# Kernel tuning notes

Measured on AMD Instinct MI355X. Metric: run time of the kernel, lower is better.

## Reference

```python
import jax, jax.numpy as jnp
import numpy as np

NUM_CLASSES = 21
TOP_K = 200
CONF_THRESH = 0.01
NMS_THRESH = 0.045
VAR0, VAR1 = 0.1, 0.2  # SSD decode variances
B, N = 128, 8732  # batch, num anchors (SSD300)


def setup_inputs() -> dict:
    key = jax.random.key(0)
    k1, k2, k3 = jax.random.split(key, 3)
    loc = jax.random.normal(k1, (B, N, 4), jnp.float32)
    conf = jax.random.normal(k2, (B, N, NUM_CLASSES), jnp.float32)
    # anchors in center-size form (cx, cy, w, h), values in (0,1)
    anchors = jax.random.uniform(k3, (N, 4), jnp.float32)
    return {"loc": loc, "conf": conf, "anchors": anchors}


def decode(loc, anchors):
    # loc [N,4], anchors [N,4] (cx,cy,w,h) -> corner boxes [N,4]
    cxcy = anchors[:, :2] + loc[:, :2] * VAR0 * anchors[:, 2:]
    wh = anchors[:, 2:] * jnp.exp(loc[:, 2:] * VAR1)
    return jnp.concatenate([cxcy - 0.5 * wh, cxcy + 0.5 * wh], axis=-1)


def pairwise_iou(boxes):
    # boxes [K,4] -> IoU [K,K]
    lt = jnp.maximum(boxes[:, None, :2], boxes[None, :, :2])
    rb = jnp.minimum(boxes[:, None, 2:], boxes[None, :, 2:])
    wh = jnp.clip(rb - lt, 0.0)
    inter = wh[..., 0] * wh[..., 1]
    area = (boxes[:, 2] - boxes[:, 0]) * (boxes[:, 3] - boxes[:, 1])
    return inter / (area[:, None] + area[None, :] - inter + 1e-12)


def nms_one_class(scores, boxes):
    # scores [N], boxes [N,4] -> packed [TOP_K, 5] (score, x1,y1,x2,y2)
    masked = jnp.where(scores > CONF_THRESH, scores, 0.0)
    top_s, idx = jax.lax.top_k(masked, TOP_K)
    top_b = boxes[idx]                      # [K,4]
    iou = pairwise_iou(top_b)               # [K,K]
    ar = jnp.arange(TOP_K)
    def body(i, keep):
        sup = keep[i] & (iou[i] > NMS_THRESH) & (ar > i)
        return keep & ~sup
    keep = jax.lax.fori_loop(0, TOP_K, body, top_s > CONF_THRESH)
    # pack kept detections to the front (stable sort preserves score order)
    order = jnp.argsort(jnp.logical_not(keep))
    ent = jnp.concatenate([top_s[:, None], top_b], axis=-1)[order]
    return jnp.where(keep[order][:, None], ent, 0.0)


def reference(loc, conf, anchors):
    probs = jax.nn.softmax(conf, axis=-1)   # [B,N,C]
    def per_image(loc_i, probs_i):
        boxes = decode(loc_i, anchors)      # [N,4]
        return jax.vmap(lambda s: nms_one_class(s, boxes))(probs_i.T)  # [C,K,5]
    out = jax.vmap(per_image)(loc, probs)   # [B,C,K,5]
    return out.at[:, 0].set(0.0)            # class 0 = background, left zero
```

## Files before the change

kernel.cpp:

```cpp
#include <hip/hip_runtime.h>
#include <math.h>

#pragma clang fp contract(off)

#define NB 128
#define NA 8732
#define NAP 8736
#define NC 21
#define TOPK 200
#define BCAP 512
#define CONF_T 0.01
#define NMS_T 0.045
#define NV (NAP / 8)
#define HSIZE 904
#define CHN 226
#define CHPAD 232
#define CH2N 29
#define KSAMP 30

__device__ __forceinline__ double exact_score_cf(const float* __restrict__ conf,
                                                 int b, int i, int c) {
  const float* row = conf + ((size_t)b * NA + i) * NC;
  float r[NC];
#pragma unroll
  for (int k = 0; k < NC; ++k) r[k] = row[k];
  float mx = r[0];
#pragma unroll
  for (int k = 1; k < NC; ++k) mx = fmaxf(mx, r[k]);
  double d = 0.0;
#pragma unroll
  for (int k = 0; k < NC; ++k) d += exp((double)r[k] - (double)mx);
  double s = exp((double)r[c] - (double)mx) / d;
  return (s > CONF_T) ? s : 0.0;
}

__device__ __forceinline__ double exact_score_aux(const float* __restrict__ conf,
                                                  const float* __restrict__ mxa,
                                                  const double* __restrict__ da,
                                                  int b, int i, int c) {
  size_t r = (size_t)b * NA + i;
  double v = (double)conf[r * NC + c];
  double m = (double)mxa[r];
  double s = exp(v - m) / da[r];
  return (s > CONF_T) ? s : 0.0;
}

__device__ __forceinline__ double exact_score(const float* __restrict__ conf,
                                              const float* __restrict__ mxa,
                                              const double* __restrict__ da,
                                              int use_aux, int b, int i, int c) {
  if (use_aux) return exact_score_aux(conf, mxa, da, b, i, c);
  return exact_score_cf(conf, b, i, c);
}

__device__ __forceinline__ void decode64(const float* __restrict__ loc,
                                         const float* __restrict__ anchors,
                                         int b, int ai, double* o) {
  const float* lp = loc + ((size_t)b * NA + ai) * 4;
  const float* ap = anchors + (size_t)ai * 4;
  double l0 = (double)lp[0], l1 = (double)lp[1];
  double l2 = (double)lp[2], l3 = (double)lp[3];
  double a0 = (double)ap[0], a1 = (double)ap[1];
  double a2 = (double)ap[2], a3 = (double)ap[3];
  double cx = a0 + (l0 * 0.1) * a2;
  double cy = a1 + (l1 * 0.1) * a3;
  double w = a2 * exp(l2 * 0.2);
  double h = a3 * exp(l3 * 0.2);
  o[0] = cx - 0.5 * w; o[1] = cy - 0.5 * h;
  o[2] = cx + 0.5 * w; o[3] = cy + 0.5 * h;
}

__device__ __forceinline__ bool entBefore(double sa, int ia, double sb, int ib) {
  return (sa > sb) || (sa == sb && ia < ib);
}

__global__ __launch_bounds__(256) void k_prep(const float* __restrict__ conf,
                                              unsigned short* __restrict__ scores,
                                              float* __restrict__ mxout,
                                              double* __restrict__ dout,
                                              int do_aux) {
  __shared__ float rows[256 * NC];
  int base = blockIdx.x * 256;
  const float4* src = (const float4*)(conf + (size_t)base * NC);
  float4* dst = (float4*)rows;
  for (int t = threadIdx.x; t < (256 * NC) / 4; t += 256) dst[t] = src[t];
  __syncthreads();
  int g = base + threadIdx.x;
  const float* row = rows + threadIdx.x * NC;
  float v[NC];
#pragma unroll
  for (int k = 0; k < NC; ++k) v[k] = row[k];
  float mx = v[0];
#pragma unroll
  for (int k = 1; k < NC; ++k) mx = fmaxf(mx, v[k]);
  float e[NC], s = 0.0f;
#pragma unroll
  for (int k = 0; k < NC; ++k) {
    e[k] = expf(v[k] - mx);
    s += e[k];
  }
  float inv = 1.0f / s;
  int b = g / NA, i = g - b * NA;
#pragma unroll
  for (int cc = 1; cc < NC; ++cc) {
    float sc = e[cc] * inv;
    scores[(size_t)(b * (NC - 1) + (cc - 1)) * NAP + i] =
        (sc > 0.0099f) ? (unsigned short)(__float_as_uint(sc) >> 16)
                       : (unsigned short)0;
  }
  if (do_aux) {
    double d = 0.0;
#pragma unroll
    for (int k = 0; k < NC; ++k) d += exp((double)v[k] - (double)mx);
    mxout[g] = mx;
    dout[g] = d;
  }
}

__global__ __launch_bounds__(256) void k_pad(unsigned short* __restrict__ scores) {
  int r = blockIdx.x * 256 + threadIdx.x;
  if (r < NB * (NC - 1)) {
    unsigned short* p = scores + (size_t)r * NAP + NA;
    p[0] = 0; p[1] = 0; p[2] = 0; p[3] = 0;
  }
}

__global__ __launch_bounds__(256, 8) void k_fast(const float* __restrict__ loc,
                                                 const float* __restrict__ conf,
                                                 const float* __restrict__ anchors,
                                                 const unsigned short* __restrict__ scores,
                                                 const float* __restrict__ mxa,
                                                 const double* __restrict__ da,
                                                 float* __restrict__ out,
                                                 int use_aux) {
  int id = blockIdx.x;
  int xcd = id & 7, slot0 = id >> 3;
  int c = slot0 % NC;
  int b = (slot0 / NC) * 8 + xcd;
  int tid = threadIdx.x;
  float* outbase = out + ((size_t)(b * NC + c)) * TOPK * 5;

  if (c == 0) {
    for (int k = tid; k < TOPK * 5; k += 256) outbase[k] = 0.0f;
    return;
  }

  __shared__ unsigned hist[HSIZE];
  __shared__ unsigned chunk[CHPAD];
  __shared__ unsigned chunk2[32];
  union U2 {
    struct { double bnds[BCAP]; int bndi[BCAP]; } bb;
    double dbox[TOPK][4];
  };
  __shared__ U2 u2;
  union U3 {
    unsigned suf[HSIZE];
    struct { float4 fbox[TOPK]; float farea[TOPK]; } fb;
  };
  __shared__ U3 u3;
  __shared__ double ssel[256];
  __shared__ int isel[256];
  __shared__ unsigned keepw[7];
  __shared__ int ctl_cnt, ctl_m, ctl_n1, ctl_kneed, ctl_lo, ctl_hi, ctl_k;
  __shared__ int ctl_fix, ctl_redo;
  __shared__ unsigned ctl_pref, ctl_L;

  const unsigned short* srow =
      scores + (size_t)(b * (NC - 1) + (c - 1)) * NAP;
  const uint4* sv = (const uint4*)srow;

  for (int t = tid; t < TOPK; t += 256) isel[t] = 0;
  if (tid < 32) chunk2[tid] = 0u;
  if (tid == 0) { ctl_cnt = 0; ctl_m = 0; ctl_fix = 0; }
  __syncthreads();
  {
    unsigned k16 = srow[tid * 34];
    if (k16) {
      int x = (int)k16 - 0x3BFF;
      if (x < 1) x = 1;
      if (x > HSIZE - 1) x = HSIZE - 1;
      atomicAdd(&chunk2[x >> 5], 1u);
    }
  }
  __syncthreads();
  if (tid == 0) {
    unsigned cum = 0;
    int w = -1;
    for (int t = CH2N - 1; t >= 0; --t) {
      cum += chunk2[t];
      if (cum >= (unsigned)KSAMP) { w = t; break; }
    }
    ctl_L = (w >= 1) ? (unsigned)(0x3BFF + (w << 5)) : 0u;
  }
  __syncthreads();

  unsigned L16x = ctl_L ? ctl_L : 1u;
  int lo, hi, n1, kneed;
  for (;;) {
    for (int t = tid; t < HSIZE; t += 256) hist[t] = 0u;
    if (tid == 0) ctl_redo = 0;
    __syncthreads();
    for (int q = tid; q < NV; q += 256) {
      uint4 v = sv[q];
      unsigned ks[8] = {v.x & 0xFFFFu, v.x >> 16, v.y & 0xFFFFu, v.y >> 16,
                        v.z & 0xFFFFu, v.z >> 16, v.w & 0xFFFFu, v.w >> 16};
#pragma unroll
      for (int t = 0; t < 8; ++t) {
        if (ks[t] >= L16x) {
          int x = (int)ks[t] - 0x3BFF;
          if (x < 1) x = 1;
          if (x > HSIZE - 1) x = HSIZE - 1;
          atomicAdd(&hist[x], 1u);
        }
      }
    }
    __syncthreads();
    if (tid < CHN) {
      unsigned csum = 0;
#pragma unroll
      for (int j = 0; j < 4; ++j) csum += hist[tid * 4 + j];
      chunk[tid] = csum;
    } else if (tid < CHPAD) {
      chunk[tid] = 0u;
    }
    __syncthreads();
    if (tid < CH2N) {
      unsigned s = 0;
#pragma unroll
      for (int j = 0; j < 8; ++j) s += chunk[tid * 8 + j];
      chunk2[tid] = s;
    }
    if (tid >= CH2N && tid < 32) chunk2[tid] = 0u;
    __syncthreads();
    if (tid == 0) {
      unsigned cum = 0;
      int t2 = -1;
      for (int t = CH2N - 1; t >= 0; --t) {
        unsigned h = chunk2[t];
        if (cum + h >= (unsigned)TOPK) { t2 = t; break; }
        cum += h;
      }
      if (t2 < 0 && L16x > 1u) {
        ctl_redo = 1;
      } else {
        if (t2 < 0) {
          ctl_lo = 1; ctl_hi = 0; ctl_n1 = (int)cum; ctl_kneed = TOPK - (int)cum;
        } else {
          int tc = t2 * 8;
          for (int t = t2 * 8 + 7; t >= t2 * 8; --t) {
            unsigned h = chunk[t];
            if (cum + h >= (unsigned)TOPK) { tc = t; break; }
            cum += h;
          }
          int D = tc * 4;
          for (int j = tc * 4 + 3; j >= tc * 4; --j) {
            unsigned h = hist[j];
            if (cum + h >= (unsigned)TOPK) { D = j; break; }
            cum += h;
          }
          int hi_ = (D + 1 < HSIZE) ? D + 1 : D;
          int lo_ = (D - 1 >= 1) ? D - 1 : D;
          unsigned hup = (hi_ > D) ? hist[hi_] : 0u;
          ctl_lo = lo_; ctl_hi = hi_;
          ctl_n1 = (int)(cum - hup);
          ctl_kneed = TOPK - ctl_n1;
        }
        unsigned run = 0;
        for (int w = CH2N - 1; w >= 0; --w) {
          unsigned h = chunk2[w];
          chunk2[w] = run;
          run += h;
        }
      }
    }
    __syncthreads();
    if (!ctl_redo) break;
    L16x = 1u;
  }
  lo = ctl_lo; hi = ctl_hi; n1 = ctl_n1; kneed = ctl_kneed;

  if (tid < CHN) {
    unsigned s = chunk2[tid >> 3];
    int ge = ((tid >> 3) + 1) << 3;
    for (int u = tid + 1; u < ge; ++u) s += chunk[u];
    int b0 = tid * 4;
    unsigned h3 = hist[b0 + 3], h2 = hist[b0 + 2], h1 = hist[b0 + 1];
    u3.suf[b0 + 3] = s;
    u3.suf[b0 + 2] = s + h3;
    u3.suf[b0 + 1] = s + h3 + h2;
    u3.suf[b0 + 0] = s + h3 + h2 + h1;
  }
  __syncthreads();

  for (int t = tid; t < HSIZE; t += 256) hist[t] = 0u;
  __syncthreads();

  {
    unsigned tC16 = (unsigned)(0x3C00 + hi);
    unsigned tB16 = (unsigned)(0x3BFF + lo);
    for (int q = tid; q < NV; q += 256) {
      uint4 v = sv[q];
      unsigned ks[8] = {v.x & 0xFFFFu, v.x >> 16, v.y & 0xFFFFu, v.y >> 16,
                        v.z & 0xFFFFu, v.z >> 16, v.w & 0xFFFFu, v.w >> 16};
#pragma unroll
      for (int t = 0; t < 8; ++t) {
        unsigned key = ks[t];
        if (key >= tC16) {
          int x = (int)key - 0x3BFF;
          if (x > HSIZE - 1) x = HSIZE - 1;
          int slot = (int)u3.suf[x] + (int)atomicAdd(&hist[x], 1u);
          if (slot < TOPK) isel[slot] = (x << 16) | (q * 8 + t);
        } else if (key >= tB16) {
          int p = atomicAdd(&ctl_m, 1);
          if (p < BCAP) u2.bb.bndi[p] = q * 8 + t;
        }
      }
    }
  }
  __syncthreads();
  int m = (hi > 0) ? ctl_m : 0;

  if (hi > 0 && m > BCAP) {
    if (tid == 0) { ctl_k = TOPK; ctl_pref = 0u; }
    __syncthreads();
    for (int shift = 8; shift >= 0; shift -= 8) {
      hist[tid] = 0u;
      __syncthreads();
      unsigned pref = ctl_pref;
      for (int q = tid; q < NV; q += 256) {
        uint4 v = sv[q];
        unsigned ks[8] = {v.x & 0xFFFFu, v.x >> 16, v.y & 0xFFFFu, v.y >> 16,
                          v.z & 0xFFFFu, v.z >> 16, v.w & 0xFFFFu, v.w >> 16};
#pragma unroll
        for (int t = 0; t < 8; ++t) {
          unsigned key = ks[t];
          if (key == 0u) continue;
          bool match = (shift == 8) || ((key >> 8) == (pref >> 8));
          if (match) atomicAdd(&hist[(key >> shift) & 255u], 1u);
        }
      }
      __syncthreads();
      if (tid == 0) {
        int k = ctl_k;
        unsigned cum = 0;
        int d = 255;
        for (; d > 0; --d) {
          unsigned h = hist[d];
          if (cum + h >= (unsigned)k) break;
          cum += h;
        }
        ctl_k = k - (int)cum;
        ctl_pref = pref | ((unsigned)d << shift);
      }
      __syncthreads();
    }
    unsigned Tf = ctl_pref;
    kneed = ctl_k;
    n1 = TOPK - kneed;
    if (tid == 0) { ctl_cnt = 0; ctl_m = 0; }
    __syncthreads();
    for (int q = tid; q < NV; q += 256) {
      uint4 v = sv[q];
      unsigned ks[8] = {v.x & 0xFFFFu, v.x >> 16, v.y & 0xFFFFu, v.y >> 16,
                        v.z & 0xFFFFu, v.z >> 16, v.w & 0xFFFFu, v.w >> 16};
#pragma unroll
      for (int t = 0; t < 8; ++t) {
        unsigned key = ks[t];
        if (key > Tf) {
          int p = atomicAdd(&ctl_cnt, 1);
          if (p < 256) isel[p] = q * 8 + t;
        } else if (key == Tf) {
          int p = atomicAdd(&ctl_m, 1);
          if (p < BCAP) u2.bb.bndi[p] = q * 8 + t;
        }
      }
    }
    __syncthreads();
    m = ctl_m;
    if (m > BCAP) m = BCAP;
    for (int q = tid; q < m; q += 256)
      u2.bb.bnds[q] = exact_score(conf, mxa, da, use_aux, b, u2.bb.bndi[q], c);
    __syncthreads();
    for (int q = tid; q < m; q += 256) {
      double sq = u2.bb.bnds[q];
      int iq = u2.bb.bndi[q];
      int rank = 0;
      for (int r = 0; r < m; ++r)
        if (entBefore(u2.bb.bnds[r], u2.bb.bndi[r], sq, iq)) ++rank;
      if (rank < kneed) { isel[n1 + rank] = iq; ssel[n1 + rank] = sq; }
    }
    __syncthreads();
    if (tid < TOPK) {
      if (tid < n1) ssel[tid] = exact_score(conf, mxa, da, use_aux, b, isel[tid], c);
    } else {
      ssel[tid] = -1.0;
      isel[tid] = 0x7fffffff;
    }
    for (int kk = 2; kk <= 256; kk <<= 1) {
      for (int j = kk >> 1; j > 0; j >>= 1) {
        __syncthreads();
        int ixj = tid ^ j;
        if (ixj > tid) {
          double s1 = ssel[tid], s2 = ssel[ixj];
          int i1 = isel[tid], i2 = isel[ixj];
          bool up = ((tid & kk) == 0);
          bool sw = up ? entBefore(s2, i2, s1, i1) : entBefore(s1, i1, s2, i2);
          if (sw) {
            ssel[tid] = s2; ssel[ixj] = s1;
            isel[tid] = i2; isel[ixj] = i1;
          }
        }
      }
    }
    __syncthreads();
  } else {
    if (tid < n1)
      ssel[tid] = exact_score(conf, mxa, da, use_aux, b, isel[tid] & 0xFFFF, c);
    if (hi > 0) {
      for (int q = tid; q < m; q += 256)
        u2.bb.bnds[q] = exact_score(conf, mxa, da, use_aux, b, u2.bb.bndi[q], c);
    }
    __syncthreads();
    double myS = 0.0;
    int myI = 0, myPos = -1;
    if (tid < n1) {
      int packed = isel[tid];
      int bk = packed >> 16;
      myI = packed & 0xFFFF;
      myS = ssel[tid];
      int base = (int)u3.suf[bk];
      int len = (int)u3.suf[bk - 1] - base;
      int r = 0;
      for (int u = base; u < base + len; ++u) {
        if (u == tid) continue;
        double ps = ssel[u];
        int pI = isel[u] & 0xFFFF;
        if (entBefore(ps, pI, myS, myI)) ++r;
      }
      myPos = base + r;
    }
    if (hi > 0) {
      for (int q = tid; q < m; q += 256) {
        double sq = u2.bb.bnds[q];
        int iq = u2.bb.bndi[q];
        int rank = 0;
        for (int r = 0; r < m; ++r)
          if (entBefore(u2.bb.bnds[r], u2.bb.bndi[r], sq, iq)) ++rank;
        if (rank < kneed) { isel[n1 + rank] = iq; ssel[n1 + rank] = sq; }
      }
    } else {
      for (int j = n1 + tid; j < TOPK; j += 256) {
        isel[j] = j - n1;
        ssel[j] = 0.0;
      }
    }
    __syncthreads();
    if (myPos >= 0 && myPos < TOPK) { ssel[myPos] = myS; isel[myPos] = myI; }
    __syncthreads();
    if (tid < 64) {
      bool inv = false;
      for (int j = tid + 1; j < TOPK; j += 64)
        if (entBefore(ssel[j], isel[j], ssel[j - 1], isel[j - 1])) inv = true;
      unsigned long long bal = __ballot((int)inv);
      if (tid == 0 && bal != 0ull) ctl_fix = 1;
    }
    __syncthreads();
    if (ctl_fix) {
      if (tid == 0) {
        for (int a = 1; a < TOPK; ++a) {
          double s = ssel[a];
          int ii = isel[a];
          int p = a - 1;
          while (p >= 0 && entBefore(s, ii, ssel[p], isel[p])) {
            ssel[p + 1] = ssel[p]; isel[p + 1] = isel[p]; --p;
          }
          ssel[p + 1] = s; isel[p + 1] = ii;
        }
      }
      __syncthreads();
    }
  }

  double dx1 = 0, dy1 = 0, dx2 = 0, dy2 = 0;
  if (tid < TOPK) {
    double bx[4];
    decode64(loc, anchors, b, isel[tid], bx);
    dx1 = bx[0]; dy1 = bx[1]; dx2 = bx[2]; dy2 = bx[3];
    u3.fb.fbox[tid] = make_float4((float)dx1, (float)dy1, (float)dx2, (float)dy2);
    u3.fb.farea[tid] = (float)((dx2 - dx1) * (dy2 - dy1));
    u2.dbox[tid][0] = dx1; u2.dbox[tid][1] = dy1;
    u2.dbox[tid][2] = dx2; u2.dbox[tid][3] = dy2;
  }
  __syncthreads();

  if (tid < 64) {
    int l = tid;
    unsigned kr = 0u;
    float4 ob[4]; float oa[4];
#pragma unroll
    for (int q = 0; q < 4; ++q) {
      int j = l + 64 * q;
      if (j < TOPK) {
        if (ssel[j] > CONF_T) kr |= 1u << q;
        ob[q] = u3.fb.fbox[j];
        oa[q] = u3.fb.farea[j];
      } else {
        ob[q] = make_float4(0.0f, 0.0f, 0.0f, 0.0f);
        oa[q] = 0.0f;
      }
    }
    int cur = 0;
    while (cur < TOPK) {
      unsigned long long ms0 = __ballot((int)(kr & 1u));
      unsigned long long ms1 = __ballot((int)(kr & 2u));
      unsigned long long ms2 = __ballot((int)(kr & 4u));
      unsigned long long ms3 = __ballot((int)(kr & 8u));
      int q0 = cur >> 6;
      int sh = cur & 63;
      unsigned long long below = sh ? ((1ull << sh) - 1ull) : 0ull;
      unsigned long long t0 = (q0 == 0) ? (ms0 & ~below) : 0ull;
      unsigned long long t1 = (q0 < 1) ? ms1 : ((q0 == 1) ? (ms1 & ~below) : 0ull);
      unsigned long long t2 = (q0 < 2) ? ms2 : ((q0 == 2) ? (ms2 & ~below) : 0ull);
      unsigned long long t3 = (q0 < 3) ? ms3 : (ms3 & ~below);
      int i = TOPK;
      if (t0) i = __ffsll(t0) - 1;
      else if (t1) i = 64 + __ffsll(t1) - 1;
      else if (t2) i = 128 + __ffsll(t2) - 1;
      else if (t3) i = 192 + __ffsll(t3) - 1;
      if (i >= TOPK) break;
      float4 fbi = u3.fb.fbox[i];
      float fai = u3.fb.farea[i];
#pragma unroll
      for (int q = 0; q < 4; ++q) {
        int r = l + 64 * q;
        if (r > i && r < TOPK && ((kr >> q) & 1u)) {
          float lx = fmaxf(fbi.x, ob[q].x), ly = fmaxf(fbi.y, ob[q].y);
          float rx = fminf(fbi.z, ob[q].z), ry = fminf(fbi.w, ob[q].w);
          float iw = fmaxf(rx - lx, 0.0f), ih = fmaxf(ry - ly, 0.0f);
          float inter = iw * ih;
          float uni = fai + oa[q] - inter + 1e-12f;
          float diff = inter - 0.045f * uni;
          bool sup;
          if (fabsf(diff) < 3e-4f * uni) {
            double ix1 = u2.dbox[i][0], iy1 = u2.dbox[i][1];
            double ix2 = u2.dbox[i][2], iy2 = u2.dbox[i][3];
            double jx1 = u2.dbox[r][0], jy1 = u2.dbox[r][1];
            double jx2 = u2.dbox[r][2], jy2 = u2.dbox[r][3];
            double dlx = fmax(ix1, jx1), dly = fmax(iy1, jy1);
            double drx = fmin(ix2, jx2), dry = fmin(iy2, jy2);
            double diw = drx - dlx; if (diw < 0.0) diw = 0.0;
            double dih = dry - dly; if (dih < 0.0) dih = 0.0;
            double dint = diw * dih;
            double dai = (ix2 - ix1) * (iy2 - iy1);
            double daj = (jx2 - jx1) * (jy2 - jy1);
            sup = dint > NMS_T * (dai + daj - dint + 1e-12);
          } else {
            sup = diff > 0.0f;
          }
          if (sup) kr &= ~(1u << q);
        }
      }
      cur = i + 1;
    }
#pragma unroll
    for (int q = 0; q < 4; ++q) {
      unsigned long long bal = __ballot((int)((kr >> q) & 1u));
      if (l == 0) {
        keepw[2 * q] = (unsigned)bal;
        if (2 * q + 1 < 7) keepw[2 * q + 1] = (unsigned)(bal >> 32);
      }
    }
  }
  __syncthreads();

  int nk = 0;
#pragma unroll
  for (int w = 0; w < 7; ++w) nk += __popc(keepw[w]);
  if (tid < TOPK) {
    int j = tid;
    bool kept = (keepw[j >> 5] >> (j & 31)) & 1u;
    if (kept) {
      int pos = 0;
      for (int w = 0; w < (j >> 5); ++w) pos += __popc(keepw[w]);
      pos += __popc(keepw[j >> 5] & ((1u << (j & 31)) - 1u));
      float* o = outbase + (size_t)pos * 5;
      o[0] = (float)ssel[j];
      o[1] = (float)dx1;
      o[2] = (float)dy1;
      o[3] = (float)dx2;
      o[4] = (float)dy2;
    }
    if (j >= nk) {
      float* o = outbase + (size_t)j * 5;
      o[0] = 0.0f; o[1] = 0.0f; o[2] = 0.0f; o[3] = 0.0f; o[4] = 0.0f;
    }
  }
}

__global__ __launch_bounds__(256) void k_main_nf(const float* __restrict__ loc,
                                                 const float* __restrict__ conf,
                                                 const float* __restrict__ anchors,
                                                 float* __restrict__ out) {
  int bc = blockIdx.x;
  int b = bc / NC;
  int c = bc % NC;
  int tid = threadIdx.x;
  float* outbase = out + (size_t)bc * TOPK * 5;
  if (c == 0) {
    for (int k = tid; k < TOPK * 5; k += 256) outbase[k] = 0.0f;
    return;
  }
  union U {
    float sf[NA];
    struct { double box[TOPK][4]; double area[TOPK]; } p2;
  };
  __shared__ U u;
  __shared__ double ssel[256];
  __shared__ int isel[256];
  __shared__ unsigned hist[256];
  __shared__ double bnds[256];
  __shared__ int bndi[256];
  __shared__ int keepL[256];
  __shared__ unsigned long long wmask[4];
  __shared__ int ctl_k, ctl_cnt, ctl_m;
  __shared__ unsigned ctl_pref;

  for (int i = tid; i < NA; i += 256)
    u.sf[i] = (float)exact_score_cf(conf, b, i, c);
  if (tid == 0) { ctl_k = TOPK; ctl_pref = 0u; }
  __syncthreads();
  for (int shift = 24; shift >= 0; shift -= 8) {
    hist[tid] = 0u;
    __syncthreads();
    unsigned pref = ctl_pref;
    for (int i = tid; i < NA; i += 256) {
      unsigned key = __float_as_uint(u.sf[i]);
      bool match = (shift == 24) || ((key >> (shift + 8)) == (pref >> (shift + 8)));
      if (match) atomicAdd(&hist[(key >> shift) & 255u], 1u);
    }
    __syncthreads();
    if (tid == 0) {
      int k = ctl_k;
      unsigned cum = 0;
      int d = 255;
      for (; d > 0; --d) {
        unsigned h = hist[d];
        if (cum + h >= (unsigned)k) break;
        cum += h;
      }
      ctl_k = k - (int)cum;
      ctl_pref = pref | ((unsigned)d << shift);
    }
    __syncthreads();
  }
  unsigned Tf = ctl_pref;
  int kneed = ctl_k;
  int n1 = TOPK - kneed;
  if (tid == 0) { ctl_cnt = 0; ctl_m = 0; }
  __syncthreads();
  for (int i = tid; i < NA; i += 256) {
    unsigned key = __float_as_uint(u.sf[i]);
    if (key > Tf) {
      int p = atomicAdd(&ctl_cnt, 1);
      if (p < 256) isel[p] = i;
    } else if (key == Tf && Tf != 0u) {
      int q = atomicAdd(&ctl_m, 1);
      if (q < 256) bndi[q] = i;
    }
  }
  __syncthreads();
  int zf;
  if (Tf == 0u) {
    zf = n1;
    for (int j = n1 + tid; j < TOPK; j += 256) isel[j] = j - n1;
  } else {
    zf = TOPK;
    int m = ctl_m;
    if (m > 256) m = 256;
    if (tid < m) bnds[tid] = exact_score_cf(conf, b, bndi[tid], c);
    __syncthreads();
    if (tid < m) {
      double sq = bnds[tid];
      int iq = bndi[tid];
      int rank = 0;
      for (int r = 0; r < m; ++r)
        if (entBefore(bnds[r], bndi[r], sq, iq)) ++rank;
      if (rank < kneed) isel[n1 + rank] = iq;
    }
  }
  __syncthreads();
  if (tid < TOPK) {
    ssel[tid] = (tid < zf) ? exact_score_cf(conf, b, isel[tid], c) : 0.0;
  } else {
    ssel[tid] = -1.0;
    isel[tid] = 0x7fffffff;
  }
  for (int kk = 2; kk <= 256; kk <<= 1) {
    for (int j = kk >> 1; j > 0; j >>= 1) {
      __syncthreads();
      int ixj = tid ^ j;
      if (ixj > tid) {
        double s1 = ssel[tid], s2 = ssel[ixj];
        int i1 = isel[tid], i2 = isel[ixj];
        bool up = ((tid & kk) == 0);
        bool sw = up ? entBefore(s2, i2, s1, i1) : entBefore(s1, i1, s2, i2);
        if (sw) {
          ssel[tid] = s2; ssel[ixj] = s1;
          isel[tid] = i2; isel[ixj] = i1;
        }
      }
    }
  }
  __syncthreads();
  if (tid < TOPK) {
    double bx[4];
    decode64(loc, anchors, b, isel[tid], bx);
    u.p2.box[tid][0] = bx[0]; u.p2.box[tid][1] = bx[1];
    u.p2.box[tid][2] = bx[2]; u.p2.box[tid][3] = bx[3];
    u.p2.area[tid] = (bx[2] - bx[0]) * (bx[3] - bx[1]);
  }
  __syncthreads();
  double mx1 = 0, my1 = 0, mx2 = 0, my2 = 0, mar = 0;
  if (tid < TOPK) {
    mx1 = u.p2.box[tid][0]; my1 = u.p2.box[tid][1];
    mx2 = u.p2.box[tid][2]; my2 = u.p2.box[tid][3];
    mar = u.p2.area[tid];
  }
  keepL[tid] = (tid < TOPK) && (ssel[tid] > CONF_T);
  __syncthreads();
  for (int i = 0; i < TOPK; ++i) {
    int ki = keepL[i];
    if (ki && tid > i && tid < TOPK && keepL[tid]) {
      double lx = fmax(u.p2.box[i][0], mx1);
      double ly = fmax(u.p2.box[i][1], my1);
      double rx = fmin(u.p2.box[i][2], mx2);
      double ry = fmin(u.p2.box[i][3], my2);
      double iw = rx - lx; if (iw < 0.0) iw = 0.0;
      double ih = ry - ly; if (ih < 0.0) ih = 0.0;
      double inter = iw * ih;
      double iou = inter / (u.p2.area[i] + mar - inter + 1e-12);
      if (iou > NMS_T) keepL[tid] = 0;
    }
    __syncthreads();
  }
  bool kj = (tid < TOPK) && (keepL[tid] != 0);
  unsigned long long bal = __ballot((int)kj);
  int wave = tid >> 6, lane = tid & 63;
  if (lane == 0) wmask[wave] = bal;
  __syncthreads();
  int nk = 0;
#pragma unroll
  for (int w = 0; w < 4; ++w) nk += __popcll(wmask[w]);
  if (kj) {
    int pos = 0;
    for (int w = 0; w < wave; ++w) pos += __popcll(wmask[w]);
    pos += __popcll(bal & ((1ull << lane) - 1ull));
    float* o = outbase + (size_t)pos * 5;
    o[0] = (float)ssel[tid];
    o[1] = (float)u.p2.box[tid][0];
    o[2] = (float)u.p2.box[tid][1];
    o[3] = (float)u.p2.box[tid][2];
    o[4] = (float)u.p2.box[tid][3];
  }
  if (tid < TOPK && tid >= nk) {
    float* o = outbase + (size_t)tid * 5;
    o[0] = 0.0f; o[1] = 0.0f; o[2] = 0.0f; o[3] = 0.0f; o[4] = 0.0f;
  }
}

extern "C" void kernel_launch(void* const* d_in, const int* in_sizes, int n_in,
                              void* d_out, int out_size, void* d_ws, size_t ws_size,
                              hipStream_t stream) {
  const float* loc = (const float*)d_in[0];
  const float* conf = (const float*)d_in[1];
  const float* anchors = (const float*)d_in[2];
  float* out = (float*)d_out;

  const size_t SC_BYTES = (size_t)NB * (NC - 1) * NAP * sizeof(unsigned short);
  const size_t MX_BYTES = (size_t)NB * NA * sizeof(float);
  const size_t D_BYTES = (size_t)NB * NA * sizeof(double);

  if (ws_size >= SC_BYTES + MX_BYTES + D_BYTES) {
    unsigned short* scores = (unsigned short*)d_ws;
    float* mxa = (float*)((char*)d_ws + SC_BYTES);
    double* da = (double*)((char*)d_ws + SC_BYTES + MX_BYTES);
    k_pad<<<10, 256, 0, stream>>>(scores);
    k_prep<<<(NB * NA) / 256, 256, 0, stream>>>(conf, scores, mxa, da, 1);
    k_fast<<<NB * NC, 256, 0, stream>>>(loc, conf, anchors, scores, mxa, da, out, 1);
  } else if (ws_size >= SC_BYTES) {
    unsigned short* scores = (unsigned short*)d_ws;
    k_pad<<<10, 256, 0, stream>>>(scores);
    k_prep<<<(NB * NA) / 256, 256, 0, stream>>>(conf, scores, nullptr, nullptr, 0);
    k_fast<<<NB * NC, 256, 0, stream>>>(loc, conf, anchors, scores, nullptr, nullptr, out, 0);
  } else {
    k_main_nf<<<NB * NC, 256, 0, stream>>>(loc, conf, anchors, out);
  }
}
```

Before: 116.9 us.

## Cache score row in registers and use wave-parallel suffix scans for threshold search

Each thread loads its share of the 16-bit score row once into registers (KREG uint4s) and reuses it across the histogram and scatter passes instead of re-reading global memory. The serial single-thread suffix scans over chunk/hist bins are replaced with wave-level shuffle suffix sums and ballots. The scatter pass now counts down from the existing histogram with atomicSub, which removes a clear and a barrier. The sampling step uses two keys per thread with a larger KSAMP, and the register cache raises VGPR pressure.

```diff
diff --git a/kernel.cpp b/kernel.cpp
--- a/kernel.cpp
+++ b/kernel.cpp
@@ -12,11 +12,12 @@
 #define CONF_T 0.01
 #define NMS_T 0.045
 #define NV (NAP / 8)
+#define KREG 5
 #define HSIZE 904
 #define CHN 226
 #define CHPAD 232
 #define CH2N 29
-#define KSAMP 30
+#define KSAMP 48
 
 __device__ __forceinline__ double exact_score_cf(const float* __restrict__ conf,
                                                  int b, int i, int c) {
@@ -72,6 +73,15 @@
 
 __device__ __forceinline__ bool entBefore(double sa, int ia, double sb, int ib) {
   return (sa > sb) || (sa == sb && ia < ib);
+}
+
+__device__ __forceinline__ unsigned wave_suffix_sum(unsigned v, int lane) {
+#pragma unroll
+  for (int off = 1; off < 64; off <<= 1) {
+    unsigned o = (unsigned)__shfl_down((int)v, off);
+    v += (lane + off < 64) ? o : 0u;
+  }
+  return v;
 }
 
 __global__ __launch_bounds__(256) void k_prep(const float* __restrict__ conf,
@@ -169,28 +179,41 @@
       scores + (size_t)(b * (NC - 1) + (c - 1)) * NAP;
   const uint4* sv = (const uint4*)srow;
 
+  uint4 kreg[KREG];
+#pragma unroll
+  for (int k = 0; k < KREG; ++k) {
+    int q = tid + 256 * k;
+    kreg[k] = (q < NV) ? sv[q] : make_uint4(0u, 0u, 0u, 0u);
+  }
   for (int t = tid; t < TOPK; t += 256) isel[t] = 0;
   if (tid < 32) chunk2[tid] = 0u;
   if (tid == 0) { ctl_cnt = 0; ctl_m = 0; ctl_fix = 0; }
   __syncthreads();
+
   {
-    unsigned k16 = srow[tid * 34];
-    if (k16) {
-      int x = (int)k16 - 0x3BFF;
+    unsigned s0 = kreg[0].x & 0xFFFFu, s1 = kreg[0].x >> 16;
+    if (s0) {
+      int x = (int)s0 - 0x3BFF;
       if (x < 1) x = 1;
       if (x > HSIZE - 1) x = HSIZE - 1;
       atomicAdd(&chunk2[x >> 5], 1u);
     }
-  }
-  __syncthreads();
-  if (tid == 0) {
-    unsigned cum = 0;
-    int w = -1;
-    for (int t = CH2N - 1; t >= 0; --t) {
-      cum += chunk2[t];
-      if (cum >= (unsigned)KSAMP) { w = t; break; }
-    }
-    ctl_L = (w >= 1) ? (unsigned)(0x3BFF + (w << 5)) : 0u;
+    if (s1) {
+      int x = (int)s1 - 0x3BFF;
+      if (x < 1) x = 1;
+      if (x > HSIZE - 1) x = HSIZE - 1;
+      atomicAdd(&chunk2[x >> 5], 1u);
+    }
+  }
+  __syncthreads();
+  if (tid < 64) {
+    unsigned h = (tid < CH2N) ? chunk2[tid] : 0u;
+    unsigned s = wave_suffix_sum(h, tid);
+    unsigned long long bal = __ballot((int)(tid < CH2N && s >= (unsigned)KSAMP));
+    if (tid == 0) {
+      int w = bal ? (63 - (int)__clzll(bal)) : -1;
+      ctl_L = (w >= 1) ? (unsigned)(0x3BFF + (w << 5)) : 0u;
+    }
   }
   __syncthreads();
 
@@ -200,17 +223,21 @@
     for (int t = tid; t < HSIZE; t += 256) hist[t] = 0u;
     if (tid == 0) ctl_redo = 0;
     __syncthreads();
-    for (int q = tid; q < NV; q += 256) {
-      uint4 v = sv[q];
-      unsigned ks[8] = {v.x & 0xFFFFu, v.x >> 16, v.y & 0xFFFFu, v.y >> 16,
-                        v.z & 0xFFFFu, v.z >> 16, v.w & 0xFFFFu, v.w >> 16};
-#pragma unroll
-      for (int t = 0; t < 8; ++t) {
-        if (ks[t] >= L16x) {
-          int x = (int)ks[t] - 0x3BFF;
-          if (x < 1) x = 1;
-          if (x > HSIZE - 1) x = HSIZE - 1;
-          atomicAdd(&hist[x], 1u);
+#pragma unroll
+    for (int k = 0; k < KREG; ++k) {
+      int q = tid + 256 * k;
+      if (q < NV) {
+        uint4 v = kreg[k];
+        unsigned ks[8] = {v.x & 0xFFFFu, v.x >> 16, v.y & 0xFFFFu, v.y >> 16,
+                          v.z & 0xFFFFu, v.z >> 16, v.w & 0xFFFFu, v.w >> 16};
+#pragma unroll
+        for (int t = 0; t < 8; ++t) {
+          if (ks[t] >= L16x) {
+            int x = (int)ks[t] - 0x3BFF;
+            if (x < 1) x = 1;
+            if (x > HSIZE - 1) x = HSIZE - 1;
+            atomicAdd(&hist[x], 1u);
+          }
         }
       }
     }
@@ -224,53 +251,50 @@
       chunk[tid] = 0u;
     }
     __syncthreads();
-    if (tid < CH2N) {
-      unsigned s = 0;
-#pragma unroll
-      for (int j = 0; j < 8; ++j) s += chunk[tid * 8 + j];
-      chunk2[tid] = s;
-    }
-    if (tid >= CH2N && tid < 32) chunk2[tid] = 0u;
-    __syncthreads();
-    if (tid == 0) {
-      unsigned cum = 0;
-      int t2 = -1;
-      for (int t = CH2N - 1; t >= 0; --t) {
-        unsigned h = chunk2[t];
-        if (cum + h >= (unsigned)TOPK) { t2 = t; break; }
-        cum += h;
-      }
+    if (tid < 64) {
+      int lane = tid;
+      unsigned h2 = 0;
+      if (lane < CH2N) {
+        int cb = lane * 8;
+#pragma unroll
+        for (int j = 0; j < 8; ++j) h2 += chunk[cb + j];
+      }
+      unsigned s2 = wave_suffix_sum(h2, lane);
+      unsigned long long bal = __ballot((int)(lane < CH2N && s2 >= (unsigned)TOPK));
+      int t2 = bal ? (63 - (int)__clzll(bal)) : -1;
       if (t2 < 0 && L16x > 1u) {
-        ctl_redo = 1;
+        if (lane == 0) ctl_redo = 1;
       } else {
         if (t2 < 0) {
-          ctl_lo = 1; ctl_hi = 0; ctl_n1 = (int)cum; ctl_kneed = TOPK - (int)cum;
+          if (lane == 0) {
+            ctl_lo = 1; ctl_hi = 0; ctl_n1 = (int)s2; ctl_kneed = TOPK - (int)s2;
+          }
         } else {
-          int tc = t2 * 8;
-          for (int t = t2 * 8 + 7; t >= t2 * 8; --t) {
-            unsigned h = chunk[t];
-            if (cum + h >= (unsigned)TOPK) { tc = t; break; }
-            cum += h;
-          }
-          int D = tc * 4;
-          for (int j = tc * 4 + 3; j >= tc * 4; --j) {
-            unsigned h = hist[j];
-            if (cum + h >= (unsigned)TOPK) { D = j; break; }
-            cum += h;
-          }
+          unsigned cumS = (unsigned)__shfl((int)(s2 - h2), t2);
+          unsigned hc = (lane < 8) ? chunk[t2 * 8 + lane] : 0u;
+          unsigned sc = wave_suffix_sum(hc, lane);
+          unsigned long long balc =
+              __ballot((int)(lane < 8 && cumS + sc >= (unsigned)TOPK));
+          int jc = 63 - (int)__clzll(balc);
+          int tc = t2 * 8 + jc;
+          unsigned cumC = cumS + (unsigned)__shfl((int)(sc - hc), jc);
+          unsigned hb = (lane < 4) ? hist[tc * 4 + lane] : 0u;
+          unsigned sb = wave_suffix_sum(hb, lane);
+          unsigned long long balb =
+              __ballot((int)(lane < 4 && cumC + sb >= (unsigned)TOPK));
+          int jb = 63 - (int)__clzll(balb);
+          int D = tc * 4 + jb;
+          unsigned cum = cumC + (unsigned)__shfl((int)(sb - hb), jb);
           int hi_ = (D + 1 < HSIZE) ? D + 1 : D;
           int lo_ = (D - 1 >= 1) ? D - 1 : D;
           unsigned hup = (hi_ > D) ? hist[hi_] : 0u;
-          ctl_lo = lo_; ctl_hi = hi_;
-          ctl_n1 = (int)(cum - hup);
-          ctl_kneed = TOPK - ctl_n1;
-        }
-        unsigned run = 0;
-        for (int w = CH2N - 1; w >= 0; --w) {
-          unsigned h = chunk2[w];
-          chunk2[w] = run;
-          run += h;
-        }
+          if (lane == 0) {
+            ctl_lo = lo_; ctl_hi = hi_;
+            ctl_n1 = (int)(cum - hup);
+            ctl_kneed = TOPK - ctl_n1;
+          }
+        }
+        if (lane < 32) chunk2[lane] = s2 - h2;
       }
     }
     __syncthreads();
@@ -292,27 +316,28 @@
   }
   __syncthreads();
 
-  for (int t = tid; t < HSIZE; t += 256) hist[t] = 0u;
-  __syncthreads();
-
   {
     unsigned tC16 = (unsigned)(0x3C00 + hi);
     unsigned tB16 = (unsigned)(0x3BFF + lo);
-    for (int q = tid; q < NV; q += 256) {
-      uint4 v = sv[q];
-      unsigned ks[8] = {v.x & 0xFFFFu, v.x >> 16, v.y & 0xFFFFu, v.y >> 16,
-                        v.z & 0xFFFFu, v.z >> 16, v.w & 0xFFFFu, v.w >> 16};
-#pragma unroll
-      for (int t = 0; t < 8; ++t) {
-        unsigned key = ks[t];
-        if (key >= tC16) {
-          int x = (int)key - 0x3BFF;
-          if (x > HSIZE - 1) x = HSIZE - 1;
-          int slot = (int)u3.suf[x] + (int)atomicAdd(&hist[x], 1u);
-          if (slot < TOPK) isel[slot] = (x << 16) | (q * 8 + t);
-        } else if (key >= tB16) {
-          int p = atomicAdd(&ctl_m, 1);
-          if (p < BCAP) u2.bb.bndi[p] = q * 8 + t;
+#pragma unroll
+    for (int k = 0; k < KREG; ++k) {
+      int q = tid + 256 * k;
+      if (q < NV) {
+        uint4 v = kreg[k];
+        unsigned ks[8] = {v.x & 0xFFFFu, v.x >> 16, v.y & 0xFFFFu, v.y >> 16,
+                          v.z & 0xFFFFu, v.z >> 16, v.w & 0xFFFFu, v.w >> 16};
+#pragma unroll
+        for (int t = 0; t < 8; ++t) {
+          unsigned key = ks[t];
+          if (key >= tC16) {
+            int x = (int)key - 0x3BFF;
+            if (x > HSIZE - 1) x = HSIZE - 1;
+            int slot = (int)u3.suf[x] + (int)atomicSub(&hist[x], 1u) - 1;
+            if (slot < TOPK) isel[slot] = (x << 16) | (q * 8 + t);
+          } else if (key >= tB16) {
+            int p = atomicAdd(&ctl_m, 1);
+            if (p < BCAP) u2.bb.bndi[p] = q * 8 + t;
+          }
         }
       }
     }
```

Result: slower. 171.0 us (+46.2%).
